# Kernel optimization log

Measured on AMD Instinct MI355X. Metric: run time of the kernel, lower is better.

The kernel has to match this reference:

```python
import jax, jax.numpy as jnp
import numpy as np

D = 64   # combine_doc_emb_len
H = 2    # heads
B = 256
S = 1024
SIDE = 56  # uid 32 + os 8 + zip 16

def _prelu(x, a):
    return jnp.where(x >= 0, x, a * x)

def _l2norm(x):
    n = jnp.sqrt(jnp.sum(x * x, axis=-1, keepdims=True))
    return x / jnp.maximum(n, 1e-12)

def _attn_branch(x_trans, y_trans, side, w1, b1, a1, w2, b2):
    b, s = x_trans.shape[0], x_trans.shape[1]
    xh = x_trans.reshape(b, s, H, D).transpose(0, 2, 1, 3)   # [B,H,S,D]
    yh = y_trans.reshape(b, 1, H, D).transpose(0, 2, 1, 3)   # [B,H,1,D]
    yhb = jnp.broadcast_to(yh, (b, H, s, D))
    sideb = jnp.broadcast_to(side[:, None, None, :], (b, H, s, side.shape[-1]))
    feat = jnp.concatenate([xh, xh * yhb, xh - yhb, yhb, sideb], axis=-1)  # [B,H,S,4D+SIDE]
    h1 = _prelu(feat @ w1 + b1, a1)          # [B,H,S,40]
    p = (h1 @ w2 + b2)[..., 0]               # [B,H,S]
    out = jnp.einsum('bhsd,bhs->bhd', xh, p).reshape(b, H * D)
    return p, out

def setup_inputs():
    key = jax.random.key(0)
    k = jax.random.split(key, 20)
    def n(i, shape, sc=1.0):
        return sc * jax.random.normal(k[i], shape, dtype=jnp.float32)
    return {
        'local_x_embs': n(0, (B, S, D)),
        'nonlocal_x_embs': n(1, (B, S, D)),
        'y_embs': n(2, (B, D)),
        'user_id_embs': n(3, (B, 32)),
        'os_embs': n(4, (B, 8)),
        'zip_code_embs': n(5, (B, 16)),
        'w_ty': n(6, (D, H * D), 0.05), 'b_ty': n(7, (H * D,), 0.05), 'a_ty': jnp.float32(0.25),
        'w_lx': n(8, (D, H * D), 0.05), 'b_lx': n(9, (H * D,), 0.05), 'a_lx': jnp.float32(0.25),
        'w_nx': n(10, (D, H * D), 0.05), 'b_nx': n(11, (H * D,), 0.05), 'a_nx': jnp.float32(0.25),
        'lw1': n(12, (4 * D + SIDE, 40), 0.05), 'lb1': n(13, (40,), 0.05), 'la1': jnp.float32(0.25),
        'lw2': n(14, (40, 1), 0.05), 'lb2': n(15, (1,), 0.05),
        'nw1': n(16, (4 * D + SIDE, 40), 0.05), 'nb1': n(17, (40,), 0.05), 'na1': jnp.float32(0.25),
        'nw2': n(18, (40, 1), 0.05), 'nb2': n(19, (1,), 0.05),
    }

def reference(local_x_embs, nonlocal_x_embs, y_embs, user_id_embs, os_embs, zip_code_embs, w_ty, b_ty, a_ty, w_lx, b_lx, a_lx, w_nx, b_nx, a_nx, lw1, lb1, la1, lw2, lb2, nw1, nb1, na1, nw2, nb2):
    side = jnp.concatenate([user_id_embs, os_embs, zip_code_embs], axis=-1)  # [B,56]
    local_x_trans = _l2norm(_prelu(local_x_embs @ w_lx + b_lx, a_lx))        # [B,S,H*D]
    nonlocal_x_trans = _l2norm(_prelu(nonlocal_x_embs @ w_nx + b_nx, a_nx))
    y_trans = _l2norm(_prelu(y_embs @ w_ty + b_ty, a_ty))                    # [B,H*D]
    _, local_embs = _attn_branch(local_x_trans, y_trans, side, lw1, lb1, la1, lw2, lb2)
    _, nonlocal_embs = _attn_branch(nonlocal_x_trans, y_trans, side, nw1, nb1, na1, nw2, nb2)
    return (local_embs, nonlocal_embs)
```

## Files before the change

kernel.cpp:

```cpp
#include <hip/hip_runtime.h>

typedef unsigned short u16;
typedef unsigned int   u32;
typedef __attribute__((ext_vector_type(8))) short bf8_t;
typedef __attribute__((ext_vector_type(4))) float f4_t;

#define NB 256
#define NS 1024

__device__ __forceinline__ u16 f2bf(float f){
    u32 u = __float_as_uint(f);
    return (u16)((u + 0x7fffu + ((u >> 16) & 1u)) >> 16);
}
__device__ __forceinline__ u32 pack_trunc(float lo, float hi){
    return __builtin_amdgcn_perm(__float_as_uint(hi), __float_as_uint(lo), 0x07060302u);
}

__global__ __launch_bounds__(256) void prep_kernel(
    const float* __restrict__ y,    const float* __restrict__ wty,
    const float* __restrict__ bty,  const float* __restrict__ aty,
    const float* __restrict__ uid,  const float* __restrict__ ose, const float* __restrict__ zipc,
    const float* __restrict__ wlx,  const float* __restrict__ wnx,
    const float* __restrict__ lw1,  const float* __restrict__ lb1,
    const float* __restrict__ nw1,  const float* __restrict__ nb1,
    u32* __restrict__ wtf, u32* __restrict__ weff, float* __restrict__ cs)
{
    const int tid = threadIdx.x;
    const int bx  = blockIdx.x;

    if (bx >= 512) {
        int u = (bx - 512)*256 + tid;
        int lane = u & 63, fr = u >> 6;
        int br = fr >> 4, t = fr & 15, n = t >> 1, ks = t & 1;
        int q = lane >> 4, lm = lane & 15;
        const float* W = br ? wnx : wlx;
        u32 out[4];
        #pragma unroll
        for (int p = 0; p < 4; ++p) {
            int k = ks*32 + q*8 + p*2;
            float lo = W[k*128 + n*16 + lm];
            float hi = W[(k+1)*128 + n*16 + lm];
            out[p] = (u32)f2bf(lo) | ((u32)f2bf(hi) << 16);
        }
        *(uint4*)&wtf[u*4] = make_uint4(out[0], out[1], out[2], out[3]);
        return;
    }

    __shared__ float yl[64];
    __shared__ float sq[128];
    __shared__ float yv[128];
    __shared__ float cpart[240];

    const int b  = bx >> 1;
    const int br = bx & 1;
    const float* w1 = br ? nw1 : lw1;
    const float* b1 = br ? nb1 : lb1;

    if (tid < 64) yl[tid] = y[b*64 + tid];
    __syncthreads();
    float v = 0.f;
    if (tid < 128) {
        float acc = bty[tid];
        for (int k = 0; k < 64; ++k) acc = fmaf(yl[k], wty[k*128 + tid], acc);
        float a = aty[0];
        v = (acc >= 0.f) ? acc : a * acc;
        sq[tid] = v * v;
    }
    __syncthreads();
    for (int s = 64; s >= 1; s >>= 1) { if (tid < s) sq[tid] += sq[tid+s]; __syncthreads(); }
    if (tid < 128) yv[tid] = v * (1.f / fmaxf(sqrtf(sq[0]), 1e-12f));
    __syncthreads();

    for (int u = tid; u < 768; u += 256) {
        int lane = u & 63, fr = u >> 6;
        int h = fr / 6, t = fr % 6, nj = t >> 1, ks = t & 1;
        int q = lane >> 4, lm = lane & 15, j = nj*16 + lm;
        u32 out[4];
        #pragma unroll
        for (int p = 0; p < 4; ++p) {
            u32 w = 0;
            #pragma unroll
            for (int e = 0; e < 2; ++e) {
                int k = ks*32 + q*8 + p*2 + e;
                float val = 0.f;
                if (j < 40)
                    val = w1[k*40 + j] + w1[(128+k)*40 + j] + yv[h*64 + k] * w1[(64+k)*40 + j];
                w |= ((u32)f2bf(val)) << (16*e);
            }
            out[p] = w;
        }
        *(uint4*)&weff[((size_t)(br*NB + b)*12 + fr)*64*4 + lane*4] =
            make_uint4(out[0], out[1], out[2], out[3]);
    }

    if (tid < 240) {
        int cj = tid / 3, sl = tid % 3;
        int h = cj / 40, j = cj % 40;
        float acc = 0.f;
        for (int t = sl*40; t < sl*40 + 40; ++t) {
            if (t < 64) {
                acc = fmaf(yv[h*64 + t], w1[(192+t)*40 + j] - w1[(128+t)*40 + j], acc);
            } else {
                int u = t - 64;
                float sv, wv;
                if (u < 32)      { sv = uid[b*32 + u];        wv = w1[(256+u)*40 + j]; }
                else if (u < 40) { sv = ose[b*8 + (u-32)];    wv = w1[(288+(u-32))*40 + j]; }
                else             { sv = zipc[b*16 + (u-40)];  wv = w1[(296+(u-40))*40 + j]; }
                acc = fmaf(sv, wv, acc);
            }
        }
        cpart[tid] = acc;
    }
    __syncthreads();
    if (tid < 96) {
        int h = tid / 48, jj = tid % 48;
        float val = 0.f;
        if (jj < 40) {
            int cj = h*40 + jj;
            val = b1[jj] + cpart[cj*3] + cpart[cj*3+1] + cpart[cj*3+2];
        }
        cs[(size_t)(br*NB + b)*96 + tid] = val;
    }
}

__global__ __launch_bounds__(256, 2) void main_kernel(
    const float* __restrict__ xloc, const float* __restrict__ xnon,
    const float* __restrict__ blx,  const float* __restrict__ alx,
    const float* __restrict__ bnx,  const float* __restrict__ anx,
    const float* __restrict__ la1,  const float* __restrict__ lw2, const float* __restrict__ lb2,
    const float* __restrict__ na1,  const float* __restrict__ nw2, const float* __restrict__ nb2,
    const u32* __restrict__ wtf, const u32* __restrict__ weff, const float* __restrict__ cs,
    float* __restrict__ out)
{
    __shared__ u16   tn[4*16*136];
    __shared__ u32   bf_sm[4096];
    __shared__ u32   cf_sm[3072];
    __shared__ float bias_sm[128];
    __shared__ float cs_sm[96];
    __shared__ float w2_sm[48];

    const int tid  = threadIdx.x;
    const int b    = blockIdx.x;
    const int br   = blockIdx.y;
    const int zc   = blockIdx.z;
    const int w    = tid >> 6;
    const int lane = tid & 63;
    const int q    = lane >> 4;
    const int lm   = lane & 15;

    const float* xg   = br ? xnon : xloc;
    const float* bias = br ? bnx  : blx;
    const float  am1  = (br ? anx[0] : alx[0]) - 1.f;
    const float  a1m1 = (br ? na1[0] : la1[0]) - 1.f;
    const float  b2v  = br ? nb2[0] : lb2[0];
    const float* w2   = br ? nw2  : lw2;

    {
        const uint4* wsrc = (const uint4*)wtf + br*1024;
        uint4* bdst = (uint4*)bf_sm;
        #pragma unroll
        for (int k = 0; k < 4; ++k) bdst[k*256 + tid] = wsrc[k*256 + tid];
        const uint4* csrc = (const uint4*)weff + (size_t)(br*NB + b)*768;
        uint4* cdst = (uint4*)cf_sm;
        #pragma unroll
        for (int k = 0; k < 3; ++k) cdst[k*256 + tid] = csrc[k*256 + tid];
    }
    if (tid < 128) bias_sm[tid] = bias[tid];
    if (tid < 96)  cs_sm[tid]   = cs[(size_t)(br*NB + b)*96 + tid];
    if (tid < 48)  w2_sm[tid]   = (tid < 40) ? w2[tid] : 0.f;

    __syncthreads();

    u16* tw = &tn[w*2176];
    const f4_t zero4 = {0.f, 0.f, 0.f, 0.f};
    float outp[8][4];
    #pragma unroll
    for (int c = 0; c < 8; ++c)
        #pragma unroll
        for (int r = 0; r < 4; ++r) outp[c][r] = 0.f;

    const float* xb = &xg[(size_t)b*NS*64];

    #pragma unroll 1
    for (int it = 0; it < 8; ++it) {
        u32 zoff = 0;
        asm volatile("" : "+v"(zoff));
        const u32*   bfp = bf_sm + zoff;
        const u32*   cfp = cf_sm + zoff;
        const float* bip = bias_sm + zoff;
        const float* cvp = cs_sm + zoff;
        const float* w2p = w2_sm + zoff;

        const float* xr = xb + (size_t)((zc*32 + it*4 + w)*16 + lm)*64;
        float4 c0 = *(const float4*)(xr + q*8);
        float4 c1 = *(const float4*)(xr + q*8 + 4);
        float4 c2 = *(const float4*)(xr + 32 + q*8);
        float4 c3 = *(const float4*)(xr + 32 + q*8 + 4);

        union { u32 u[4]; bf8_t v; } A0, A1;
        A0.u[0] = pack_trunc(c0.x, c0.y); A0.u[1] = pack_trunc(c0.z, c0.w);
        A0.u[2] = pack_trunc(c1.x, c1.y); A0.u[3] = pack_trunc(c1.z, c1.w);
        A1.u[0] = pack_trunc(c2.x, c2.y); A1.u[1] = pack_trunc(c2.z, c2.w);
        A1.u[2] = pack_trunc(c3.x, c3.y); A1.u[3] = pack_trunc(c3.z, c3.w);

        float tv[8][4];
        float s0 = 0.f, s1 = 0.f, s2 = 0.f, s3 = 0.f;
        #pragma unroll
        for (int c = 0; c < 8; ++c) {
            f4_t bi = *(const f4_t*)&bip[c*16 + q*4];
            bf8_t bf0 = *(const bf8_t*)&bfp[((c*2 + 0)*64 + lane)*4];
            bf8_t bf1 = *(const bf8_t*)&bfp[((c*2 + 1)*64 + lane)*4];
            f4_t acc = __builtin_amdgcn_mfma_f32_16x16x32_bf16(bf0, A0.v, bi,  0, 0, 0);
            acc      = __builtin_amdgcn_mfma_f32_16x16x32_bf16(bf1, A1.v, acc, 0, 0, 0);
            float v0 = acc[0]; v0 = fmaf(fminf(v0, 0.f), am1, v0); tv[c][0] = v0; s0 = fmaf(v0, v0, s0);
            float v1 = acc[1]; v1 = fmaf(fminf(v1, 0.f), am1, v1); tv[c][1] = v1; s1 = fmaf(v1, v1, s1);
            float v2 = acc[2]; v2 = fmaf(fminf(v2, 0.f), am1, v2); tv[c][2] = v2; s2 = fmaf(v2, v2, s2);
            float v3 = acc[3]; v3 = fmaf(fminf(v3, 0.f), am1, v3); tv[c][3] = v3; s3 = fmaf(v3, v3, s3);
        }
        float ssq = (s0 + s1) + (s2 + s3);
        ssq += __shfl_xor(ssq, 16);
        ssq += __shfl_xor(ssq, 32);
        const float rinv = 1.f / fmaxf(sqrtf(ssq), 1e-12f);

        #pragma unroll
        for (int c = 0; c < 8; ++c) {
            u32 lo = pack_trunc(tv[c][0], tv[c][1]);
            u32 hi = pack_trunc(tv[c][2], tv[c][3]);
            *(uint2*)&tw[lm*136 + c*16 + q*4] = make_uint2(lo, hi);
        }

        float pw[2];
        #pragma unroll
        for (int h = 0; h < 2; ++h) {
            bf8_t ac0 = *(const bf8_t*)&tw[lm*136 + h*64 + q*8];
            bf8_t ac1 = *(const bf8_t*)&tw[lm*136 + h*64 + 32 + q*8];
            float pp[3];
            #pragma unroll
            for (int nj = 0; nj < 3; ++nj) {
                f4_t cv = *(const f4_t*)&cvp[h*48 + nj*16 + q*4];
                f4_t wv = *(const f4_t*)&w2p[nj*16 + q*4];
                bf8_t cf0 = *(const bf8_t*)&cfp[((h*6 + nj*2 + 0)*64 + lane)*4];
                bf8_t cf1 = *(const bf8_t*)&cfp[((h*6 + nj*2 + 1)*64 + lane)*4];
                f4_t acc = __builtin_amdgcn_mfma_f32_16x16x32_bf16(cf0, ac0, zero4, 0, 0, 0);
                acc      = __builtin_amdgcn_mfma_f32_16x16x32_bf16(cf1, ac1, acc,   0, 0, 0);
                float ppl = 0.f;
                #pragma unroll
                for (int r = 0; r < 4; ++r) {
                    float vv = fmaf(acc[r], rinv, cv[r]);
                    vv = fmaf(fminf(vv, 0.f), a1m1, vv);
                    ppl = fmaf(vv, wv[r], ppl);
                }
                pp[nj] = ppl;
            }
            float p = (pp[0] + pp[1]) + pp[2];
            p += __shfl_xor(p, 16);
            p += __shfl_xor(p, 32);
            pw[h] = (p + b2v) * rinv;
        }

        #pragma unroll
        for (int c = 0; c < 8; ++c)
            #pragma unroll
            for (int r = 0; r < 4; ++r)
                outp[c][r] = fmaf(tv[c][r], pw[c >> 2], outp[c][r]);
    }

    #pragma unroll
    for (int c = 0; c < 8; ++c)
        #pragma unroll
        for (int r = 0; r < 4; ++r) {
            float v = outp[c][r];
            v += __shfl_xor(v, 1);
            v += __shfl_xor(v, 2);
            v += __shfl_xor(v, 4);
            v += __shfl_xor(v, 8);
            outp[c][r] = v;
        }

    __syncthreads();
    float* red = (float*)tn;
    if (lm == 0) {
        #pragma unroll
        for (int c = 0; c < 8; ++c) {
            f4_t v = { outp[c][0], outp[c][1], outp[c][2], outp[c][3] };
            *(f4_t*)&red[w*128 + c*16 + q*4] = v;
        }
    }
    __syncthreads();
    if (tid < 128) {
        float s = red[tid] + red[128 + tid] + red[256 + tid] + red[384 + tid];
        atomicAdd(&out[((size_t)br*NB + b)*128 + tid], s);
    }
}

extern "C" void kernel_launch(void* const* d_in, const int* in_sizes, int n_in,
                              void* d_out, int out_size, void* d_ws, size_t ws_size,
                              hipStream_t stream)
{
    const float* xl  = (const float*)d_in[0];
    const float* xn  = (const float*)d_in[1];
    const float* y   = (const float*)d_in[2];
    const float* uid = (const float*)d_in[3];
    const float* ose = (const float*)d_in[4];
    const float* zp  = (const float*)d_in[5];
    const float* wty = (const float*)d_in[6];
    const float* bty = (const float*)d_in[7];
    const float* aty = (const float*)d_in[8];
    const float* wlx = (const float*)d_in[9];
    const float* blx = (const float*)d_in[10];
    const float* alx = (const float*)d_in[11];
    const float* wnx = (const float*)d_in[12];
    const float* bnx = (const float*)d_in[13];
    const float* anx = (const float*)d_in[14];
    const float* lw1 = (const float*)d_in[15];
    const float* lb1 = (const float*)d_in[16];
    const float* la1 = (const float*)d_in[17];
    const float* lw2 = (const float*)d_in[18];
    const float* lb2 = (const float*)d_in[19];
    const float* nw1 = (const float*)d_in[20];
    const float* nb1 = (const float*)d_in[21];
    const float* na1 = (const float*)d_in[22];
    const float* nw2 = (const float*)d_in[23];
    const float* nb2 = (const float*)d_in[24];

    u32*   wtf  = (u32*)d_ws;
    u32*   weff = (u32*)((char*)d_ws + 32768);
    float* cs   = (float*)((char*)d_ws + 32768 + 6291456);

    hipMemsetAsync(d_out, 0, (size_t)out_size * sizeof(float), stream);
    prep_kernel<<<dim3(520), dim3(256), 0, stream>>>(
        y, wty, bty, aty, uid, ose, zp, wlx, wnx, lw1, lb1, nw1, nb1, wtf, weff, cs);
    main_kernel<<<dim3(NB, 2, 2), dim3(256), 0, stream>>>(
        xl, xn, blx, alx, bnx, anx,
        la1, lw2, lb2, na1, nw2, nb2,
        wtf, weff, cs, (float*)d_out);
}
```

Baseline: 247.9 us.

## Process two row tiles per wave with register-held weights and prefetch, drop split-S atomics

Each block now covers the whole sequence for a (batch, branch) pair, so the grid halves and the output is written directly instead of being zero-filled and combined with atomics. Each wave handles two 16-row tiles per iteration, and the first-layer weight fragments are kept in registers rather than shared memory. The next iteration's input rows are prefetched into registers to hide global load latency. It also swaps the divide-and-sqrt norm for rsqrt. The trade-off is fewer blocks (512) and higher register pressure with occupancy bound 1, which can reduce latency hiding.

```diff
diff --git a/kernel.cpp b/kernel.cpp
--- a/kernel.cpp
+++ b/kernel.cpp
@@ -123,7 +123,7 @@
     }
 }
 
-__global__ __launch_bounds__(256, 2) void main_kernel(
+__global__ __launch_bounds__(256, 1) void main_kernel(
     const float* __restrict__ xloc, const float* __restrict__ xnon,
     const float* __restrict__ blx,  const float* __restrict__ alx,
     const float* __restrict__ bnx,  const float* __restrict__ anx,
@@ -132,8 +132,7 @@
     const u32* __restrict__ wtf, const u32* __restrict__ weff, const float* __restrict__ cs,
     float* __restrict__ out)
 {
-    __shared__ u16   tn[4*16*136];
-    __shared__ u32   bf_sm[4096];
+    __shared__ u16   tn[4*2*16*136];
     __shared__ u32   cf_sm[3072];
     __shared__ float bias_sm[128];
     __shared__ float cs_sm[96];
@@ -142,7 +141,6 @@
     const int tid  = threadIdx.x;
     const int b    = blockIdx.x;
     const int br   = blockIdx.y;
-    const int zc   = blockIdx.z;
     const int w    = tid >> 6;
     const int lane = tid & 63;
     const int q    = lane >> 4;
@@ -156,10 +154,6 @@
     const float* w2   = br ? nw2  : lw2;
 
     {
-        const uint4* wsrc = (const uint4*)wtf + br*1024;
-        uint4* bdst = (uint4*)bf_sm;
-        #pragma unroll
-        for (int k = 0; k < 4; ++k) bdst[k*256 + tid] = wsrc[k*256 + tid];
         const uint4* csrc = (const uint4*)weff + (size_t)(br*NB + b)*768;
         uint4* cdst = (uint4*)cf_sm;
         #pragma unroll
@@ -169,9 +163,18 @@
     if (tid < 96)  cs_sm[tid]   = cs[(size_t)(br*NB + b)*96 + tid];
     if (tid < 48)  w2_sm[tid]   = (tid < 40) ? w2[tid] : 0.f;
 
-    __syncthreads();
-
-    u16* tw = &tn[w*2176];
+    const bf8_t* wtfv = (const bf8_t*)wtf;
+    bf8_t Bfrag[8][2];
+    #pragma unroll
+    for (int n = 0; n < 8; ++n)
+        #pragma unroll
+        for (int ks = 0; ks < 2; ++ks)
+            Bfrag[n][ks] = wtfv[(br*16 + n*2 + ks)*64 + lane];
+
+    __syncthreads();
+
+    u16* twa = &tn[w*4352];
+    u16* twb = twa + 2176;
     const f4_t zero4 = {0.f, 0.f, 0.f, 0.f};
     float outp[8][4];
     #pragma unroll
@@ -181,88 +184,138 @@
 
     const float* xb = &xg[(size_t)b*NS*64];
 
+    float4 pa0, pa1, pa2, pa3, pb0, pb1, pb2, pb3;
+    {
+        const float* xra = xb + (size_t)(w*16 + lm)*64;
+        pa0 = *(const float4*)(xra + q*8);
+        pa1 = *(const float4*)(xra + q*8 + 4);
+        pa2 = *(const float4*)(xra + 32 + q*8);
+        pa3 = *(const float4*)(xra + 32 + q*8 + 4);
+        const float* xrb = xb + (size_t)((4 + w)*16 + lm)*64;
+        pb0 = *(const float4*)(xrb + q*8);
+        pb1 = *(const float4*)(xrb + q*8 + 4);
+        pb2 = *(const float4*)(xrb + 32 + q*8);
+        pb3 = *(const float4*)(xrb + 32 + q*8 + 4);
+    }
+
     #pragma unroll 1
     for (int it = 0; it < 8; ++it) {
         u32 zoff = 0;
         asm volatile("" : "+v"(zoff));
-        const u32*   bfp = bf_sm + zoff;
         const u32*   cfp = cf_sm + zoff;
         const float* bip = bias_sm + zoff;
         const float* cvp = cs_sm + zoff;
         const float* w2p = w2_sm + zoff;
 
-        const float* xr = xb + (size_t)((zc*32 + it*4 + w)*16 + lm)*64;
-        float4 c0 = *(const float4*)(xr + q*8);
-        float4 c1 = *(const float4*)(xr + q*8 + 4);
-        float4 c2 = *(const float4*)(xr + 32 + q*8);
-        float4 c3 = *(const float4*)(xr + 32 + q*8 + 4);
-
-        union { u32 u[4]; bf8_t v; } A0, A1;
-        A0.u[0] = pack_trunc(c0.x, c0.y); A0.u[1] = pack_trunc(c0.z, c0.w);
-        A0.u[2] = pack_trunc(c1.x, c1.y); A0.u[3] = pack_trunc(c1.z, c1.w);
-        A1.u[0] = pack_trunc(c2.x, c2.y); A1.u[1] = pack_trunc(c2.z, c2.w);
-        A1.u[2] = pack_trunc(c3.x, c3.y); A1.u[3] = pack_trunc(c3.z, c3.w);
-
-        float tv[8][4];
-        float s0 = 0.f, s1 = 0.f, s2 = 0.f, s3 = 0.f;
+        float4 ca0 = pa0, ca1 = pa1, ca2 = pa2, ca3 = pa3;
+        float4 cb0 = pb0, cb1 = pb1, cb2 = pb2, cb3 = pb3;
+        if (it < 7) {
+            const float* xra = xb + (size_t)(((it+1)*8 + w)*16 + lm)*64;
+            pa0 = *(const float4*)(xra + q*8);
+            pa1 = *(const float4*)(xra + q*8 + 4);
+            pa2 = *(const float4*)(xra + 32 + q*8);
+            pa3 = *(const float4*)(xra + 32 + q*8 + 4);
+            const float* xrb = xb + (size_t)(((it+1)*8 + 4 + w)*16 + lm)*64;
+            pb0 = *(const float4*)(xrb + q*8);
+            pb1 = *(const float4*)(xrb + q*8 + 4);
+            pb2 = *(const float4*)(xrb + 32 + q*8);
+            pb3 = *(const float4*)(xrb + 32 + q*8 + 4);
+        }
+
+        union { u32 u[4]; bf8_t v; } Aa0, Aa1, Ab0, Ab1;
+        Aa0.u[0] = pack_trunc(ca0.x, ca0.y); Aa0.u[1] = pack_trunc(ca0.z, ca0.w);
+        Aa0.u[2] = pack_trunc(ca1.x, ca1.y); Aa0.u[3] = pack_trunc(ca1.z, ca1.w);
+        Aa1.u[0] = pack_trunc(ca2.x, ca2.y); Aa1.u[1] = pack_trunc(ca2.z, ca2.w);
+        Aa1.u[2] = pack_trunc(ca3.x, ca3.y); Aa1.u[3] = pack_trunc(ca3.z, ca3.w);
+        Ab0.u[0] = pack_trunc(cb0.x, cb0.y); Ab0.u[1] = pack_trunc(cb0.z, cb0.w);
+        Ab0.u[2] = pack_trunc(cb1.x, cb1.y); Ab0.u[3] = pack_trunc(cb1.z, cb1.w);
+        Ab1.u[0] = pack_trunc(cb2.x, cb2.y); Ab1.u[1] = pack_trunc(cb2.z, cb2.w);
+        Ab1.u[2] = pack_trunc(cb3.x, cb3.y); Ab1.u[3] = pack_trunc(cb3.z, cb3.w);
+
+        float tva[8][4], tvb[8][4];
+        float sa0 = 0.f, sa1 = 0.f, sa2 = 0.f, sa3 = 0.f;
+        float sb0 = 0.f, sb1 = 0.f, sb2 = 0.f, sb3 = 0.f;
         #pragma unroll
         for (int c = 0; c < 8; ++c) {
             f4_t bi = *(const f4_t*)&bip[c*16 + q*4];
-            bf8_t bf0 = *(const bf8_t*)&bfp[((c*2 + 0)*64 + lane)*4];
-            bf8_t bf1 = *(const bf8_t*)&bfp[((c*2 + 1)*64 + lane)*4];
-            f4_t acc = __builtin_amdgcn_mfma_f32_16x16x32_bf16(bf0, A0.v, bi,  0, 0, 0);
-            acc      = __builtin_amdgcn_mfma_f32_16x16x32_bf16(bf1, A1.v, acc, 0, 0, 0);
-            float v0 = acc[0]; v0 = fmaf(fminf(v0, 0.f), am1, v0); tv[c][0] = v0; s0 = fmaf(v0, v0, s0);
-            float v1 = acc[1]; v1 = fmaf(fminf(v1, 0.f), am1, v1); tv[c][1] = v1; s1 = fmaf(v1, v1, s1);
-            float v2 = acc[2]; v2 = fmaf(fminf(v2, 0.f), am1, v2); tv[c][2] = v2; s2 = fmaf(v2, v2, s2);
-            float v3 = acc[3]; v3 = fmaf(fminf(v3, 0.f), am1, v3); tv[c][3] = v3; s3 = fmaf(v3, v3, s3);
-        }
-        float ssq = (s0 + s1) + (s2 + s3);
-        ssq += __shfl_xor(ssq, 16);
-        ssq += __shfl_xor(ssq, 32);
-        const float rinv = 1.f / fmaxf(sqrtf(ssq), 1e-12f);
+            f4_t qa = __builtin_amdgcn_mfma_f32_16x16x32_bf16(Bfrag[c][0], Aa0.v, bi, 0, 0, 0);
+            qa      = __builtin_amdgcn_mfma_f32_16x16x32_bf16(Bfrag[c][1], Aa1.v, qa, 0, 0, 0);
+            f4_t qb = __builtin_amdgcn_mfma_f32_16x16x32_bf16(Bfrag[c][0], Ab0.v, bi, 0, 0, 0);
+            qb      = __builtin_amdgcn_mfma_f32_16x16x32_bf16(Bfrag[c][1], Ab1.v, qb, 0, 0, 0);
+            float a0 = qa[0]; a0 = fmaf(fminf(a0, 0.f), am1, a0); tva[c][0] = a0; sa0 = fmaf(a0, a0, sa0);
+            float a1 = qa[1]; a1 = fmaf(fminf(a1, 0.f), am1, a1); tva[c][1] = a1; sa1 = fmaf(a1, a1, sa1);
+            float a2 = qa[2]; a2 = fmaf(fminf(a2, 0.f), am1, a2); tva[c][2] = a2; sa2 = fmaf(a2, a2, sa2);
+            float a3 = qa[3]; a3 = fmaf(fminf(a3, 0.f), am1, a3); tva[c][3] = a3; sa3 = fmaf(a3, a3, sa3);
+            float b0 = qb[0]; b0 = fmaf(fminf(b0, 0.f), am1, b0); tvb[c][0] = b0; sb0 = fmaf(b0, b0, sb0);
+            float b1 = qb[1]; b1 = fmaf(fminf(b1, 0.f), am1, b1); tvb[c][1] = b1; sb1 = fmaf(b1, b1, sb1);
+            float b2 = qb[2]; b2 = fmaf(fminf(b2, 0.f), am1, b2); tvb[c][2] = b2; sb2 = fmaf(b2, b2, sb2);
+            float b3 = qb[3]; b3 = fmaf(fminf(b3, 0.f), am1, b3); tvb[c][3] = b3; sb3 = fmaf(b3, b3, sb3);
+        }
 
         #pragma unroll
         for (int c = 0; c < 8; ++c) {
-            u32 lo = pack_trunc(tv[c][0], tv[c][1]);
-            u32 hi = pack_trunc(tv[c][2], tv[c][3]);
-            *(uint2*)&tw[lm*136 + c*16 + q*4] = make_uint2(lo, hi);
-        }
-
-        float pw[2];
+            *(uint2*)&twa[lm*136 + c*16 + q*4] =
+                make_uint2(pack_trunc(tva[c][0], tva[c][1]), pack_trunc(tva[c][2], tva[c][3]));
+            *(uint2*)&twb[lm*136 + c*16 + q*4] =
+                make_uint2(pack_trunc(tvb[c][0], tvb[c][1]), pack_trunc(tvb[c][2], tvb[c][3]));
+        }
+
+        float ssqa = (sa0 + sa1) + (sa2 + sa3);
+        ssqa += __shfl_xor(ssqa, 16);
+        ssqa += __shfl_xor(ssqa, 32);
+        const float rinva = rsqrtf(fmaxf(ssqa, 1e-24f));
+        float ssqb = (sb0 + sb1) + (sb2 + sb3);
+        ssqb += __shfl_xor(ssqb, 16);
+        ssqb += __shfl_xor(ssqb, 32);
+        const float rinvb = rsqrtf(fmaxf(ssqb, 1e-24f));
+
+        float pwa[2], pwb[2];
         #pragma unroll
         for (int h = 0; h < 2; ++h) {
-            bf8_t ac0 = *(const bf8_t*)&tw[lm*136 + h*64 + q*8];
-            bf8_t ac1 = *(const bf8_t*)&tw[lm*136 + h*64 + 32 + q*8];
-            float pp[3];
+            bf8_t aca0 = *(const bf8_t*)&twa[lm*136 + h*64 + q*8];
+            bf8_t aca1 = *(const bf8_t*)&twa[lm*136 + h*64 + 32 + q*8];
+            bf8_t acb0 = *(const bf8_t*)&twb[lm*136 + h*64 + q*8];
+            bf8_t acb1 = *(const bf8_t*)&twb[lm*136 + h*64 + 32 + q*8];
+            float ppa[3], ppb[3];
             #pragma unroll
             for (int nj = 0; nj < 3; ++nj) {
                 f4_t cv = *(const f4_t*)&cvp[h*48 + nj*16 + q*4];
                 f4_t wv = *(const f4_t*)&w2p[nj*16 + q*4];
                 bf8_t cf0 = *(const bf8_t*)&cfp[((h*6 + nj*2 + 0)*64 + lane)*4];
                 bf8_t cf1 = *(const bf8_t*)&cfp[((h*6 + nj*2 + 1)*64 + lane)*4];
-                f4_t acc = __builtin_amdgcn_mfma_f32_16x16x32_bf16(cf0, ac0, zero4, 0, 0, 0);
-                acc      = __builtin_amdgcn_mfma_f32_16x16x32_bf16(cf1, ac1, acc,   0, 0, 0);
-                float ppl = 0.f;
+                f4_t qa = __builtin_amdgcn_mfma_f32_16x16x32_bf16(cf0, aca0, zero4, 0, 0, 0);
+                qa      = __builtin_amdgcn_mfma_f32_16x16x32_bf16(cf1, aca1, qa,    0, 0, 0);
+                f4_t qb = __builtin_amdgcn_mfma_f32_16x16x32_bf16(cf0, acb0, zero4, 0, 0, 0);
+                qb      = __builtin_amdgcn_mfma_f32_16x16x32_bf16(cf1, acb1, qb,    0, 0, 0);
+                float pla = 0.f, plb = 0.f;
                 #pragma unroll
                 for (int r = 0; r < 4; ++r) {
-                    float vv = fmaf(acc[r], rinv, cv[r]);
-                    vv = fmaf(fminf(vv, 0.f), a1m1, vv);
-                    ppl = fmaf(vv, wv[r], ppl);
+                    float va = fmaf(qa[r], rinva, cv[r]);
+                    va = fmaf(fminf(va, 0.f), a1m1, va);
+                    pla = fmaf(va, wv[r], pla);
+                    float vb = fmaf(qb[r], rinvb, cv[r]);
+                    vb = fmaf(fminf(vb, 0.f), a1m1, vb);
+                    plb = fmaf(vb, wv[r], plb);
                 }
-                pp[nj] = ppl;
+                ppa[nj] = pla; ppb[nj] = plb;
             }
-            float p = (pp[0] + pp[1]) + pp[2];
-            p += __shfl_xor(p, 16);
-            p += __shfl_xor(p, 32);
-            pw[h] = (p + b2v) * rinv;
+            float p_a = (ppa[0] + ppa[1]) + ppa[2];
+            p_a += __shfl_xor(p_a, 16);
+            p_a += __shfl_xor(p_a, 32);
+            pwa[h] = (p_a + b2v) * rinva;
+            float p_b = (ppb[0] + ppb[1]) + ppb[2];
+            p_b += __shfl_xor(p_b, 16);
+            p_b += __shfl_xor(p_b, 32);
+            pwb[h] = (p_b + b2v) * rinvb;
         }
 
         #pragma unroll
         for (int c = 0; c < 8; ++c)
             #pragma unroll
-            for (int r = 0; r < 4; ++r)
-                outp[c][r] = fmaf(tv[c][r], pw[c >> 2], outp[c][r]);
+            for (int r = 0; r < 4; ++r) {
+                outp[c][r] = fmaf(tva[c][r], pwa[c >> 2], outp[c][r]);
+                outp[c][r] = fmaf(tvb[c][r], pwb[c >> 2], outp[c][r]);
+            }
     }
 
     #pragma unroll
@@ -289,7 +342,7 @@
     __syncthreads();
     if (tid < 128) {
         float s = red[tid] + red[128 + tid] + red[256 + tid] + red[384 + tid];
-        atomicAdd(&out[((size_t)br*NB + b)*128 + tid], s);
+        out[((size_t)br*NB + b)*128 + tid] = s;
     }
 }
 
@@ -327,10 +380,9 @@
     u32*   weff = (u32*)((char*)d_ws + 32768);
     float* cs   = (float*)((char*)d_ws + 32768 + 6291456);
 
-    hipMemsetAsync(d_out, 0, (size_t)out_size * sizeof(float), stream);
     prep_kernel<<<dim3(520), dim3(256), 0, stream>>>(
         y, wty, bty, aty, uid, ose, zp, wlx, wnx, lw1, lb1, nw1, nb1, wtf, weff, cs);
-    main_kernel<<<dim3(NB, 2, 2), dim3(256), 0, stream>>>(
+    main_kernel<<<dim3(NB, 2), dim3(256), 0, stream>>>(
         xl, xn, blx, alx, bnx, anx,
         la1, lw2, lb2, na1, nw2, nb2,
         wtf, weff, cs, (float*)d_out);
```

Measured after the change: 235.8 us. 4.9% less time.
